# Optimization experiments

Hardware: AMD Instinct MI355X
Metric: run time of the kernel (lower is better)

Reference implementation:

```python
import jax, jax.numpy as jnp
import numpy as np

BIG = 1e9
GRAPH_LAYERS = 2
FLOW_ITERS = 10
DUAL_ITERS = 10
STEP = 0.1
MOM = 0.9


def _forward(node_features, node_embeddings, demands, adj, neighborhoods,
             enc_W0, enc_b0, enc_W1, enc_b1,
             attn_W, attn_a_src, attn_a_dst, nbr_q,
             gru_W, gru_U, gru_b,
             dec_W0, dec_b0, dec_W1, dec_b1,
             dual_W0, dual_b0, dual_W1, dual_b1):
    E = enc_W1.shape[1]
    K = neighborhoods.shape[0]
    # --- node encoder MLP (tanh, activate_final=True) ---
    x = jnp.concatenate([node_embeddings, node_features], axis=-1)  # [B,N,Fin]
    h = jnp.tanh(jnp.tanh(x @ enc_W0 + enc_b0) @ enc_W1 + enc_b1)   # [B,N,E]
    attn_coefs = None
    for _ in range(GRAPH_LAYERS):
        # --- AttentionNeighborhood: multi-head GAT per hop level, then attention over levels ---
        z = jnp.einsum('bnd,hde->hbne', h, attn_W)                   # [H,B,N,E]
        s_src = jnp.einsum('hbne,he->hbn', z, attn_a_src)
        s_dst = jnp.einsum('hbne,he->hbn', z, attn_a_dst)
        scores = jnp.tanh(s_src[:, :, :, None] + s_dst[:, :, None, :])  # [H,B,N,N]
        aggs = []
        for k in range(K):
            masked = jnp.where(neighborhoods[k][None] > 0, scores, -BIG)
            alpha = jax.nn.softmax(masked, axis=-1)                  # [H,B,N,N]
            agg = jnp.tanh(jnp.einsum('hbnm,hbme->hbne', alpha, z).mean(axis=0))  # heads averaged -> [B,N,E]
            aggs.append(agg)
        aggs = jnp.stack(aggs, axis=2)                               # [B,N,K,E]
        attn_coefs = jax.nn.softmax(jnp.tanh(jnp.einsum('bnke,e->bnk', aggs, nbr_q)), axis=-1)
        nxt = jnp.einsum('bnk,bnke->bne', attn_coefs, aggs)          # [B,N,E]
        # --- GRU state update (tanh activation) ---
        zr = jax.nn.sigmoid(nxt @ gru_W[:, :2 * E] + h @ gru_U[:, :2 * E] + gru_b[:2 * E])
        zg, r = zr[..., :E], zr[..., E:]
        h_tilde = jnp.tanh(nxt @ gru_W[:, 2 * E:] + (r * h) @ gru_U[:, 2 * E:] + gru_b[2 * E:])
        h = (1.0 - zg) * h + zg * h_tilde
    # --- flow-proportion decoder + masked softmax over neighbors ---
    node_weights = jnp.tanh(h @ dec_W0 + dec_b0) @ dec_W1 + dec_b1   # [B,N,1]
    pred = adj * jnp.swapaxes(node_weights, 1, 2)                    # adj * node_weights^T
    weights = -BIG * (1.0 - adj) + pred
    prop = jax.nn.softmax(weights, axis=-1)                          # [B,N,N]
    # --- iterative min-cost-flow solver ---
    def mcf_step(flow, _):
        inflow = flow.sum(axis=1)[:, :, None]                        # inflow_i = sum_j flow[j,i]
        return prop * jax.nn.relu(inflow - demands), None
    flow, _ = jax.lax.scan(mcf_step, jnp.zeros_like(prop), None, length=FLOW_ITERS)
    # should_correct_flows: cancel opposing flow on each edge pair
    flow = flow - adj * jnp.minimum(flow, jnp.swapaxes(flow, 1, 2))
    flow_cost = jnp.sum(flow * flow, axis=(1, 2))                    # square cost, per graph
    # --- dual decoder + projected momentum ascent dual-flow solver ---
    dual_vars = jnp.tanh(h @ dual_W0 + dual_b0) @ dual_W1 + dual_b1  # [B,N,1]
    dual_diff = adj * (dual_vars - jnp.swapaxes(dual_vars, 1, 2))    # [B,N,N]
    def dual_step(carry, _):
        y, m = carry
        g = 2.0 * y - dual_diff                                      # d/dy [y^2 - dual_diff*y]
        m = MOM * m + g
        y = adj * jax.nn.relu(y - STEP * m)
        return (y, m), None
    (dflow, _m), _ = jax.lax.scan(dual_step,
                                  (jnp.zeros_like(dual_diff), jnp.zeros_like(dual_diff)),
                                  None, length=DUAL_ITERS)
    dual_demand = jnp.sum(dual_vars * demands, axis=(1, 2))
    dual_cost = jnp.sum(dflow * dflow - dual_diff * dflow, axis=(1, 2)) - dual_demand
    return flow_cost - dual_cost                                     # primal-dual gap loss, [B]


def setup_inputs() -> dict:
    key = jax.random.key(0)
    ks = jax.random.split(key, 24)
    B, N, Femb, Ffeat, E, H = 2, 2048, 16, 2, 64, 2
    Fin = Femb + Ffeat
    node_embeddings = jax.random.normal(ks[0], (B, N, Femb), jnp.float32)
    node_features = jax.random.normal(ks[1], (B, N, Ffeat), jnp.float32)
    d = jax.random.normal(ks[2], (B, N, 1), jnp.float32) * 0.1
    demands = d - d.mean(axis=1, keepdims=True)                      # balanced demands
    eye = jnp.eye(N, dtype=jnp.float32)
    u = jax.random.uniform(ks[3], (B, N, N))
    adj = (u < 0.008).astype(jnp.float32) * (1.0 - eye)              # avg degree ~16
    a2 = (jnp.matmul(adj, adj) > 0).astype(jnp.float32) * (1.0 - eye)
    neighborhoods = jnp.stack([adj, a2], axis=0)                     # [K,B,N,N]
    def init(k, fan_in, shape):
        return jax.random.normal(k, shape, jnp.float32) / jnp.sqrt(float(fan_in))
    return {
        'node_features': node_features, 'node_embeddings': node_embeddings,
        'demands': demands, 'adj': adj, 'neighborhoods': neighborhoods,
        'enc_W0': init(ks[4], Fin, (Fin, 64)), 'enc_b0': jnp.zeros((64,)),
        'enc_W1': init(ks[5], 64, (64, E)), 'enc_b1': jnp.zeros((E,)),
        'attn_W': init(ks[6], E, (H, E, E)),
        'attn_a_src': init(ks[7], E, (H, E)), 'attn_a_dst': init(ks[8], E, (H, E)),
        'nbr_q': init(ks[9], E, (E,)),
        'gru_W': init(ks[10], E, (E, 3 * E)), 'gru_U': init(ks[11], E, (E, 3 * E)),
        'gru_b': jnp.zeros((3 * E,)),
        'dec_W0': init(ks[12], E, (E, 64)), 'dec_b0': jnp.zeros((64,)),
        'dec_W1': init(ks[13], 64, (64, 1)), 'dec_b1': jnp.zeros((1,)),
        'dual_W0': init(ks[14], E, (E, 64)), 'dual_b0': jnp.zeros((64,)),
        'dual_W1': init(ks[15], 64, (64, 1)), 'dual_b1': jnp.zeros((1,)),
    }


def reference(node_features, node_embeddings, demands, adj, neighborhoods,
              enc_W0, enc_b0, enc_W1, enc_b1,
              attn_W, attn_a_src, attn_a_dst, nbr_q,
              gru_W, gru_U, gru_b,
              dec_W0, dec_b0, dec_W1, dec_b1,
              dual_W0, dual_b0, dual_W1, dual_b1):
    return _forward(node_features, node_embeddings, demands, adj, neighborhoods,
                    enc_W0, enc_b0, enc_W1, enc_b1,
                    attn_W, attn_a_src, attn_a_dst, nbr_q,
                    gru_W, gru_U, gru_b,
                    dec_W0, dec_b0, dec_W1, dec_b1,
                    dual_W0, dual_b0, dual_W1, dual_b1)
```

## Files before the change

### kernel.cpp

```cpp
#include <hip/hip_runtime.h>

#define B_ 2
#define N_ 2048
#define E_ 64
#define FIN_ 18
#define ADJ_CAP 128
#define A2_CAP 1024
#define DR 16

__device__ __forceinline__ float wave_sum(float v) {
  #pragma unroll
  for (int o = 32; o > 0; o >>= 1) v += __shfl_xor(v, o);
  return v;
}
__device__ __forceinline__ float wave_max(float v) {
  #pragma unroll
  for (int o = 32; o > 0; o >>= 1) v = fmaxf(v, __shfl_xor(v, o));
  return v;
}
__device__ __forceinline__ void grp_reduce(float4& a) {
  #pragma unroll
  for (int o = 16; o <= 32; o <<= 1) {
    a.x += __shfl_xor(a.x, o); a.y += __shfl_xor(a.y, o);
    a.z += __shfl_xor(a.z, o); a.w += __shfl_xor(a.w, o);
  }
}

__global__ void k_csr(const float* __restrict__ nbhd, int* __restrict__ adj_idx,
                      int* __restrict__ adj_cnt, int* __restrict__ a2_idx,
                      int* __restrict__ a2_cnt, float* __restrict__ accum) {
  int wid = blockIdx.x * 4 + (threadIdx.x >> 6);
  int lane = threadIdx.x & 63;
  if (wid == 0 && lane < 8) accum[lane] = 0.f;
  int k = wid / (B_ * N_);
  int rem = wid - k * (B_ * N_);
  const float* row = nbhd + ((size_t)k * (B_ * N_) + rem) * N_;
  int cap = (k == 0) ? ADJ_CAP : A2_CAP;
  int* idx = ((k == 0) ? adj_idx : a2_idx) + (size_t)rem * cap;
  int* cntp = ((k == 0) ? adj_cnt : a2_cnt) + rem;
  int cnt = 0;
  unsigned long long below = (1ull << lane) - 1ull;
  for (int j0 = 0; j0 < N_; j0 += 256) {
    float4 v = ((const float4*)(row + j0))[lane];
    bool p0 = v.x > 0.f, p1 = v.y > 0.f, p2 = v.z > 0.f, p3 = v.w > 0.f;
    unsigned long long b0 = __ballot(p0), b1 = __ballot(p1),
                       b2 = __ballot(p2), b3 = __ballot(p3);
    int pos = cnt + __popcll(b0 & below) + __popcll(b1 & below) +
              __popcll(b2 & below) + __popcll(b3 & below);
    int base_j = j0 + lane * 4;
    if (p0) { if (pos < cap) idx[pos] = base_j;     pos++; }
    if (p1) { if (pos < cap) idx[pos] = base_j + 1; pos++; }
    if (p2) { if (pos < cap) idx[pos] = base_j + 2; pos++; }
    if (p3) { if (pos < cap) idx[pos] = base_j + 3; pos++; }
    cnt += __popcll(b0) + __popcll(b1) + __popcll(b2) + __popcll(b3);
  }
  if (lane == 0) *cntp = (cnt < cap) ? cnt : cap;
}

__global__ __launch_bounds__(256) void k_enc(
    const float* __restrict__ emb, const float* __restrict__ feat,
    const float* __restrict__ W0, const float* __restrict__ b0,
    const float* __restrict__ W1, const float* __restrict__ b1,
    float* __restrict__ h) {
  int tid = threadIdx.x, w = tid >> 6, j = tid & 63;
  int row0 = blockIdx.x * DR;
  __shared__ float XL[DR][FIN_];
  __shared__ float HID[DR][64];
  for (int t = tid; t < DR * FIN_; t += 256) {
    int r = t / FIN_, d = t - r * FIN_;
    int row = row0 + r;
    XL[r][d] = (d < 16) ? emb[(size_t)row * 16 + d] : feat[(size_t)row * 2 + (d - 16)];
  }
  __syncthreads();
  float acc[4];
  float b0j = b0[j];
  #pragma unroll
  for (int r = 0; r < 4; r++) acc[r] = b0j;
  #pragma unroll 2
  for (int d = 0; d < FIN_; d++) {
    float wv = W0[d * 64 + j];
    #pragma unroll
    for (int r = 0; r < 4; r++) acc[r] += XL[w * 4 + r][d] * wv;
  }
  #pragma unroll
  for (int r = 0; r < 4; r++) HID[w * 4 + r][j] = tanhf(acc[r]);
  float b1j = b1[j];
  #pragma unroll
  for (int r = 0; r < 4; r++) acc[r] = b1j;
  for (int dq = 0; dq < 16; dq++) {
    float w0 = W1[(4 * dq + 0) * 64 + j];
    float w1 = W1[(4 * dq + 1) * 64 + j];
    float w2 = W1[(4 * dq + 2) * 64 + j];
    float w3 = W1[(4 * dq + 3) * 64 + j];
    #pragma unroll
    for (int r = 0; r < 4; r++) {
      float4 x = ((const float4*)HID[w * 4 + r])[dq];
      acc[r] += x.x * w0 + x.y * w1 + x.z * w2 + x.w * w3;
    }
  }
  #pragma unroll
  for (int r = 0; r < 4; r++)
    h[(size_t)(row0 + w * 4 + r) * 64 + j] = tanhf(acc[r]);
}

__global__ __launch_bounds__(256) void k_z(
    const float* __restrict__ h, const float* __restrict__ attn_W,
    const float* __restrict__ a_src, const float* __restrict__ a_dst,
    float* __restrict__ z, float* __restrict__ ssrc2, float* __restrict__ sdst2) {
  int tid = threadIdx.x, w = tid >> 6, j = tid & 63;
  int head = w & 1, rbase = (w >> 1) * 8;
  int row0 = blockIdx.x * DR;
  __shared__ float HL[DR][64];
  for (int t = tid; t < DR * 64; t += 256) HL[t >> 6][t & 63] = h[(size_t)row0 * 64 + t];
  __syncthreads();
  const float* W = attn_W + head * 64 * 64;
  float acc[8];
  #pragma unroll
  for (int r = 0; r < 8; r++) acc[r] = 0.f;
  for (int dq = 0; dq < 16; dq++) {
    float w0 = W[(4 * dq + 0) * 64 + j];
    float w1 = W[(4 * dq + 1) * 64 + j];
    float w2 = W[(4 * dq + 2) * 64 + j];
    float w3 = W[(4 * dq + 3) * 64 + j];
    #pragma unroll
    for (int r = 0; r < 8; r++) {
      float4 x = ((const float4*)HL[rbase + r])[dq];
      acc[r] += x.x * w0 + x.y * w1 + x.z * w2 + x.w * w3;
    }
  }
  float as = a_src[head * 64 + j], ad = a_dst[head * 64 + j];
  #pragma unroll
  for (int r = 0; r < 8; r++) {
    int row = row0 + rbase + r;
    z[((size_t)head * (B_ * N_) + row) * 64 + j] = acc[r];
    float rs = wave_sum(acc[r] * as), rd = wave_sum(acc[r] * ad);
    if (j == 0) {
      ssrc2[(size_t)row * 2 + head] = rs;
      sdst2[(size_t)row * 2 + head] = rd;
    }
  }
}

__global__ __launch_bounds__(64) void k_agg_adj(
    const int* __restrict__ adj_idx, const int* __restrict__ adj_cnt,
    const float* __restrict__ z, const float* __restrict__ ssrc2,
    const float* __restrict__ sdst2, float* __restrict__ aggs) {
  int row = blockIdx.x;
  int lane = threadIdx.x;
  int b = row >> 11;
  int cnt = adj_cnt[row];
  const int* idx = adj_idx + (size_t)row * ADJ_CAP;
  float2 ss = ((const float2*)ssrc2)[row];
  const float2* sd = (const float2*)sdst2 + (size_t)b * N_;
  int col0 = 0, col1 = 0;
  float e00 = 0.f, e10 = 0.f, e01 = 0.f, e11 = 0.f;
  if (lane < cnt) {
    col0 = idx[lane]; float2 s = sd[col0];
    e00 = __expf(tanhf(ss.x + s.x)); e10 = __expf(tanhf(ss.y + s.y));
  }
  if (lane + 64 < cnt) {
    col1 = idx[lane + 64]; float2 s = sd[col1];
    e01 = __expf(tanhf(ss.x + s.x)); e11 = __expf(tanhf(ss.y + s.y));
  }
  float tot0 = wave_sum(e00 + e01), tot1 = wave_sum(e10 + e11);
  float inv0 = (tot0 > 0.f) ? 1.f / tot0 : 0.f;
  float inv1 = (tot1 > 0.f) ? 1.f / tot1 : 0.f;
  const float* z0 = z + (size_t)b * N_ * 64;
  const float* z1 = z + ((size_t)(B_ * N_) + b * N_) * 64;
  int g = lane >> 4, li = lane & 15;
  float4 a0 = {0.f, 0.f, 0.f, 0.f}, a1 = {0.f, 0.f, 0.f, 0.f};
  for (int j0 = 0; j0 < 64; j0 += 4) {
    if (j0 >= cnt) break;
    int j = j0 + g;
    int c = __shfl(col0, j);
    float e0 = __shfl(e00, j), e1 = __shfl(e10, j);
    if (j < cnt) {
      float4 v0 = ((const float4*)(z0 + (size_t)c * 64))[li];
      float4 v1 = ((const float4*)(z1 + (size_t)c * 64))[li];
      a0.x += e0 * v0.x; a0.y += e0 * v0.y; a0.z += e0 * v0.z; a0.w += e0 * v0.w;
      a1.x += e1 * v1.x; a1.y += e1 * v1.y; a1.z += e1 * v1.z; a1.w += e1 * v1.w;
    }
  }
  if (cnt > 64) {
    for (int j0 = 0; j0 < 64; j0 += 4) {
      if (64 + j0 >= cnt) break;
      int j = j0 + g;
      int c = __shfl(col1, j);
      float e0 = __shfl(e01, j), e1 = __shfl(e11, j);
      if (64 + j < cnt) {
        float4 v0 = ((const float4*)(z0 + (size_t)c * 64))[li];
        float4 v1 = ((const float4*)(z1 + (size_t)c * 64))[li];
        a0.x += e0 * v0.x; a0.y += e0 * v0.y; a0.z += e0 * v0.z; a0.w += e0 * v0.w;
        a1.x += e1 * v1.x; a1.y += e1 * v1.y; a1.z += e1 * v1.z; a1.w += e1 * v1.w;
      }
    }
  }
  grp_reduce(a0); grp_reduce(a1);
  if (g == 0) {
    float4 o;
    o.x = tanhf(0.5f * (a0.x * inv0 + a1.x * inv1));
    o.y = tanhf(0.5f * (a0.y * inv0 + a1.y * inv1));
    o.z = tanhf(0.5f * (a0.z * inv0 + a1.z * inv1));
    o.w = tanhf(0.5f * (a0.w * inv0 + a1.w * inv1));
    ((float4*)(aggs + ((size_t)row * 2 + 0) * 64))[li] = o;
  }
}

__global__ __launch_bounds__(256) void k_agg_a2(
    const int* __restrict__ a2_idx, const int* __restrict__ a2_cnt,
    const float* __restrict__ z, const float* __restrict__ ssrc2,
    const float* __restrict__ sdst2, float* __restrict__ aggs) {
  int row = blockIdx.x;
  int tid = threadIdx.x;
  int w = tid >> 6, lane = tid & 63;
  int b = row >> 11;
  int cnt = a2_cnt[row];
  const int* idx = a2_idx + (size_t)row * A2_CAP;
  float2 ss = ((const float2*)ssrc2)[row];
  const float2* sd = (const float2*)sdst2 + (size_t)b * N_;
  int colr[4]; float e0r[4], e1r[4];
  float s0 = 0.f, s1 = 0.f;
  #pragma unroll
  for (int c = 0; c < 4; c++) {
    int t = c * 256 + tid;
    colr[c] = 0; e0r[c] = 0.f; e1r[c] = 0.f;
    if (t < cnt) {
      int cc = idx[t]; colr[c] = cc;
      float2 s = sd[cc];
      e0r[c] = __expf(tanhf(ss.x + s.x));
      e1r[c] = __expf(tanhf(ss.y + s.y));
      s0 += e0r[c]; s1 += e1r[c];
    }
  }
  s0 = wave_sum(s0); s1 = wave_sum(s1);
  __shared__ float RED[2][4];
  __shared__ float WS0[4][64], WS1[4][64];
  if (lane == 0) { RED[0][w] = s0; RED[1][w] = s1; }
  const float* z0 = z + (size_t)b * N_ * 64;
  const float* z1 = z + ((size_t)(B_ * N_) + b * N_) * 64;
  int g = lane >> 4, li = lane & 15;
  float4 a0 = {0.f, 0.f, 0.f, 0.f}, a1 = {0.f, 0.f, 0.f, 0.f};
  #pragma unroll
  for (int c = 0; c < 4; c++) {
    int base = c * 256 + w * 64;
    if (base >= cnt) break;
    for (int j0 = 0; j0 < 64; j0 += 4) {
      if (base + j0 >= cnt) break;
      int j = j0 + g;
      int col = __shfl(colr[c], j);
      float e0 = __shfl(e0r[c], j), e1 = __shfl(e1r[c], j);
      if (base + j < cnt) {
        float4 v0 = ((const float4*)(z0 + (size_t)col * 64))[li];
        float4 v1 = ((const float4*)(z1 + (size_t)col * 64))[li];
        a0.x += e0 * v0.x; a0.y += e0 * v0.y; a0.z += e0 * v0.z; a0.w += e0 * v0.w;
        a1.x += e1 * v1.x; a1.y += e1 * v1.y; a1.z += e1 * v1.z; a1.w += e1 * v1.w;
      }
    }
  }
  grp_reduce(a0); grp_reduce(a1);
  if (g == 0) {
    ((float4*)WS0[w])[li] = a0;
    ((float4*)WS1[w])[li] = a1;
  }
  __syncthreads();
  if (tid < 64) {
    float tot0 = RED[0][0] + RED[0][1] + RED[0][2] + RED[0][3];
    float tot1 = RED[1][0] + RED[1][1] + RED[1][2] + RED[1][3];
    float inv0 = (tot0 > 0.f) ? 1.f / tot0 : 0.f;
    float inv1 = (tot1 > 0.f) ? 1.f / tot1 : 0.f;
    float r0 = WS0[0][tid] + WS0[1][tid] + WS0[2][tid] + WS0[3][tid];
    float r1 = WS1[0][tid] + WS1[1][tid] + WS1[2][tid] + WS1[3][tid];
    aggs[((size_t)row * 2 + 1) * 64 + tid] = tanhf(0.5f * (r0 * inv0 + r1 * inv1));
  }
}

__global__ __launch_bounds__(256) void k_comb(
    const float* __restrict__ aggs, const float* __restrict__ nbr_q,
    const float* __restrict__ gru_W, const float* __restrict__ gru_U,
    const float* __restrict__ gru_b, float* __restrict__ h) {
  int tid = threadIdx.x, w = tid >> 6, j = tid & 63;
  int row0 = blockIdx.x * DR;
  __shared__ float HL[DR][64], NL[DR][64], RGL[DR][64];
  for (int t = tid; t < DR * 64; t += 256) HL[t >> 6][t & 63] = h[(size_t)row0 * 64 + t];
  float q = nbr_q[j];
  #pragma unroll
  for (int r = 0; r < 4; r++) {
    int rr = w * 4 + r, row = row0 + rr;
    float a0 = aggs[((size_t)row * 2 + 0) * 64 + j];
    float a1 = aggs[((size_t)row * 2 + 1) * 64 + j];
    float t0 = tanhf(wave_sum(a0 * q));
    float t1 = tanhf(wave_sum(a1 * q));
    float mx = fmaxf(t0, t1);
    float e0 = __expf(t0 - mx), e1 = __expf(t1 - mx);
    float inv = 1.f / (e0 + e1);
    NL[rr][j] = (e0 * a0 + e1 * a1) * inv;
  }
  __syncthreads();
  float az[4], ar[4];
  float bz = gru_b[j], br = gru_b[64 + j];
  #pragma unroll
  for (int r = 0; r < 4; r++) { az[r] = bz; ar[r] = br; }
  for (int dq = 0; dq < 16; dq++) {
    int d0 = 4 * dq;
    float wz0 = gru_W[(d0 + 0) * 192 + j],      wz1 = gru_W[(d0 + 1) * 192 + j];
    float wz2 = gru_W[(d0 + 2) * 192 + j],      wz3 = gru_W[(d0 + 3) * 192 + j];
    float wr0 = gru_W[(d0 + 0) * 192 + 64 + j], wr1 = gru_W[(d0 + 1) * 192 + 64 + j];
    float wr2 = gru_W[(d0 + 2) * 192 + 64 + j], wr3 = gru_W[(d0 + 3) * 192 + 64 + j];
    float uz0 = gru_U[(d0 + 0) * 192 + j],      uz1 = gru_U[(d0 + 1) * 192 + j];
    float uz2 = gru_U[(d0 + 2) * 192 + j],      uz3 = gru_U[(d0 + 3) * 192 + j];
    float ur0 = gru_U[(d0 + 0) * 192 + 64 + j], ur1 = gru_U[(d0 + 1) * 192 + 64 + j];
    float ur2 = gru_U[(d0 + 2) * 192 + 64 + j], ur3 = gru_U[(d0 + 3) * 192 + 64 + j];
    #pragma unroll
    for (int r = 0; r < 4; r++) {
      float4 n = ((const float4*)NL[w * 4 + r])[dq];
      float4 x = ((const float4*)HL[w * 4 + r])[dq];
      az[r] += n.x * wz0 + n.y * wz1 + n.z * wz2 + n.w * wz3
             + x.x * uz0 + x.y * uz1 + x.z * uz2 + x.w * uz3;
      ar[r] += n.x * wr0 + n.y * wr1 + n.z * wr2 + n.w * wr3
             + x.x * ur0 + x.y * ur1 + x.z * ur2 + x.w * ur3;
    }
  }
  float zgr[4];
  #pragma unroll
  for (int r = 0; r < 4; r++) {
    zgr[r] = 1.f / (1.f + __expf(-az[r]));
    RGL[w * 4 + r][j] = 1.f / (1.f + __expf(-ar[r]));
  }
  float ah[4];
  float bh = gru_b[128 + j];
  #pragma unroll
  for (int r = 0; r < 4; r++) ah[r] = bh;
  for (int dq = 0; dq < 16; dq++) {
    int d0 = 4 * dq;
    float wh0 = gru_W[(d0 + 0) * 192 + 128 + j], wh1 = gru_W[(d0 + 1) * 192 + 128 + j];
    float wh2 = gru_W[(d0 + 2) * 192 + 128 + j], wh3 = gru_W[(d0 + 3) * 192 + 128 + j];
    float uh0 = gru_U[(d0 + 0) * 192 + 128 + j], uh1 = gru_U[(d0 + 1) * 192 + 128 + j];
    float uh2 = gru_U[(d0 + 2) * 192 + 128 + j], uh3 = gru_U[(d0 + 3) * 192 + 128 + j];
    #pragma unroll
    for (int r = 0; r < 4; r++) {
      float4 n = ((const float4*)NL[w * 4 + r])[dq];
      float4 x = ((const float4*)HL[w * 4 + r])[dq];
      float4 rg = ((const float4*)RGL[w * 4 + r])[dq];
      ah[r] += n.x * wh0 + n.y * wh1 + n.z * wh2 + n.w * wh3
             + rg.x * x.x * uh0 + rg.y * x.y * uh1
             + rg.z * x.z * uh2 + rg.w * x.w * uh3;
    }
  }
  #pragma unroll
  for (int r = 0; r < 4; r++) {
    int rr = w * 4 + r;
    float ht = tanhf(ah[r]);
    float hj = HL[rr][j];
    h[(size_t)(row0 + rr) * 64 + j] = (1.f - zgr[r]) * hj + zgr[r] * ht;
  }
}

__global__ __launch_bounds__(256) void k_dec(
    const float* __restrict__ h, const float* __restrict__ dW0,
    const float* __restrict__ db0, const float* __restrict__ dW1,
    const float* __restrict__ db1, const float* __restrict__ uW0,
    const float* __restrict__ ub0, const float* __restrict__ uW1,
    const float* __restrict__ ub1, const float* __restrict__ demands,
    float* __restrict__ nw, float* __restrict__ dv, float* accum) {
  int tid = threadIdx.x, w = tid >> 6, j = tid & 63;
  int row0 = blockIdx.x * DR;
  __shared__ float HL[DR][64];
  __shared__ float DD[4];
  for (int t = tid; t < DR * 64; t += 256) HL[t >> 6][t & 63] = h[(size_t)row0 * 64 + t];
  __syncthreads();
  float accd[4], accu[4];
  float db0j = db0[j], ub0j = ub0[j];
  #pragma unroll
  for (int r = 0; r < 4; r++) { accd[r] = db0j; accu[r] = ub0j; }
  for (int dq = 0; dq < 16; dq++) {
    int d0 = 4 * dq;
    float dw0 = dW0[(d0 + 0) * 64 + j], dw1 = dW0[(d0 + 1) * 64 + j];
    float dw2 = dW0[(d0 + 2) * 64 + j], dw3 = dW0[(d0 + 3) * 64 + j];
    float uw0 = uW0[(d0 + 0) * 64 + j], uw1 = uW0[(d0 + 1) * 64 + j];
    float uw2 = uW0[(d0 + 2) * 64 + j], uw3 = uW0[(d0 + 3) * 64 + j];
    #pragma unroll
    for (int r = 0; r < 4; r++) {
      float4 x = ((const float4*)HL[w * 4 + r])[dq];
      accd[r] += x.x * dw0 + x.y * dw1 + x.z * dw2 + x.w * dw3;
      accu[r] += x.x * uw0 + x.y * uw1 + x.z * uw2 + x.w * uw3;
    }
  }
  float dw1c = dW1[j], uw1c = uW1[j];
  float db1s = db1[0], ub1s = ub1[0];
  float ddl = 0.f;
  #pragma unroll
  for (int r = 0; r < 4; r++) {
    int row = row0 + w * 4 + r;
    float a = wave_sum(tanhf(accd[r]) * dw1c);
    float bb = wave_sum(tanhf(accu[r]) * uw1c);
    if (j == 0) {
      float dvv = bb + ub1s;
      nw[row] = a + db1s; dv[row] = dvv;
      ddl += dvv * demands[row];
    }
  }
  if (j == 0) DD[w] = ddl;
  __syncthreads();
  if (tid == 0) atomicAdd(&accum[4 + (row0 >> 11)], DD[0] + DD[1] + DD[2] + DD[3]);
}

__global__ void k_prop(const int* __restrict__ adj_idx, const int* __restrict__ adj_cnt,
                       const float* __restrict__ nw, float* __restrict__ Pval,
                       int* __restrict__ tcnt) {
  int row = blockIdx.x;
  int lane = threadIdx.x;
  int b = row >> 11;
  int cnt = adj_cnt[row];
  const int* idx = adj_idx + (size_t)row * ADJ_CAP;
  int c0 = (lane < cnt) ? idx[lane] : -1;
  int c1 = (lane + 64 < cnt) ? idx[lane + 64] : -1;
  float v0 = (c0 >= 0) ? nw[b * N_ + c0] : -1e30f;
  float v1 = (c1 >= 0) ? nw[b * N_ + c1] : -1e30f;
  float m = wave_max(fmaxf(v0, v1));
  float e0 = (c0 >= 0) ? __expf(v0 - m) : 0.f;
  float e1 = (c1 >= 0) ? __expf(v1 - m) : 0.f;
  float s = wave_sum(e0 + e1);
  float inv = (s > 0.f) ? 1.f / s : 0.f;
  if (c0 >= 0) Pval[(size_t)row * ADJ_CAP + lane] = e0 * inv;
  if (c1 >= 0) Pval[(size_t)row * ADJ_CAP + lane + 64] = e1 * inv;
  if (lane == 0) tcnt[row] = 0;
}

__global__ void k_transpose(const int* __restrict__ adj_idx, const int* __restrict__ adj_cnt,
                            const float* __restrict__ Pval, int* __restrict__ tcnt,
                            int* __restrict__ tsrc, float* __restrict__ tval) {
  int row = blockIdx.x;
  int lane = threadIdx.x;
  int cnt = adj_cnt[row];
  int base = row & ~(N_ - 1);
  for (int t = lane; t < cnt; t += 64) {
    int j = adj_idx[(size_t)row * ADJ_CAP + t];
    int col = base + j;
    int pos = atomicAdd(&tcnt[col], 1);
    if (pos < ADJ_CAP) {
      tsrc[(size_t)col * ADJ_CAP + pos] = row;
      tval[(size_t)col * ADJ_CAP + pos] = Pval[(size_t)row * ADJ_CAP + t];
    }
  }
}

__global__ __launch_bounds__(1024) void k_mcf_all(
    const int* __restrict__ tcnt, const int* __restrict__ tsrc,
    const float* __restrict__ tval, const float* __restrict__ demands,
    float* __restrict__ s_out) {
  int b = blockIdx.x, tid = threadIdx.x;
  __shared__ float SBUF[2][N_];
  __shared__ float DL[N_];
  for (int i = tid; i < N_; i += 1024) {
    float d = demands[b * N_ + i];
    DL[i] = d;
    SBUF[0][i] = fmaxf(-d, 0.f);
  }
  __syncthreads();
  int cur = 0;
  for (int it = 0; it < 9; it++) {
    const float* Sin = SBUF[cur];
    float* Sout = SBUF[cur ^ 1];
    for (int i = tid; i < N_; i += 1024) {
      int gi = b * N_ + i;
      int cnt = tcnt[gi];
      const int* src = tsrc + (size_t)gi * ADJ_CAP;
      const float* val = tval + (size_t)gi * ADJ_CAP;
      float c = 0.f;
      int c4 = cnt >> 2;
      for (int qq = 0; qq < c4; qq++) {
        int4 s4 = ((const int4*)src)[qq];
        float4 v4 = ((const float4*)val)[qq];
        c += v4.x * Sin[s4.x & (N_ - 1)] + v4.y * Sin[s4.y & (N_ - 1)]
           + v4.z * Sin[s4.z & (N_ - 1)] + v4.w * Sin[s4.w & (N_ - 1)];
      }
      for (int t = c4 * 4; t < cnt; t++) c += val[t] * Sin[src[t] & (N_ - 1)];
      Sout[i] = fmaxf(c - DL[i], 0.f);
    }
    __syncthreads();
    cur ^= 1;
  }
  for (int i = tid; i < N_; i += 1024) s_out[b * N_ + i] = SBUF[cur][i];
}

__global__ __launch_bounds__(256) void k_flowdual(
    const int* __restrict__ adj_idx, const int* __restrict__ adj_cnt,
    const float* __restrict__ Pval, const float* __restrict__ s,
    const float* __restrict__ dv, float* accum) {
  int tid = threadIdx.x;
  int lane = tid & 63, w = tid >> 6;
  int r16 = lane >> 4, e = lane & 15;
  int row = blockIdx.x * 16 + w * 4 + r16;
  int b = row >> 11, i = row & (N_ - 1);
  int cnt = adj_cnt[row];
  float si = s[row], dvi = dv[row];
  const int* idx = adj_idx + (size_t)row * ADJ_CAP;
  const float* pv = Pval + (size_t)row * ADJ_CAP;
  float fc = 0.f, dc = 0.f;
  for (int t = e; t < cnt; t += 16) {
    int j = idx[t];
    float f_ij = si * pv[t];
    const int* jidx = adj_idx + (size_t)(b * N_ + j) * ADJ_CAP;
    int jcnt = adj_cnt[b * N_ + j];
    int lo = 0, hi = jcnt, pos = -1;
    while (lo < hi) {
      int mid = (lo + hi) >> 1;
      int v = jidx[mid];
      if (v == i) { pos = mid; break; }
      if (v < i) lo = mid + 1; else hi = mid;
    }
    float f_ji = (pos >= 0) ? s[b * N_ + j] * Pval[(size_t)(b * N_ + j) * ADJ_CAP + pos] : 0.f;
    float fin = f_ij - fminf(f_ij, f_ji);
    fc += fin * fin;
    float dd = dvi - dv[b * N_ + j];
    float y = 0.f, m = 0.f;
    #pragma unroll
    for (int q = 0; q < 10; q++) {
      float g = 2.f * y - dd;
      m = 0.9f * m + g;
      y = fmaxf(y - 0.1f * m, 0.f);
    }
    dc += y * y - dd * y;
  }
  fc = wave_sum(fc); dc = wave_sum(dc);
  __shared__ float FB[4], DB[4];
  if (lane == 0) { FB[w] = fc; DB[w] = dc; }
  __syncthreads();
  if (tid == 0) {
    int bb = (blockIdx.x * 16) >> 11;
    atomicAdd(&accum[bb], FB[0] + FB[1] + FB[2] + FB[3]);
    atomicAdd(&accum[2 + bb], DB[0] + DB[1] + DB[2] + DB[3]);
  }
}

__global__ void k_fin(const float* accum, float* out) {
  int b = threadIdx.x;
  if (b < B_) out[b] = accum[b] - accum[2 + b] + accum[4 + b];
}

extern "C" void kernel_launch(void* const* d_in, const int* in_sizes, int n_in,
                              void* d_out, int out_size, void* d_ws, size_t ws_size,
                              hipStream_t stream) {
  const float* feat    = (const float*)d_in[0];
  const float* emb     = (const float*)d_in[1];
  const float* demands = (const float*)d_in[2];
  const float* nbhd    = (const float*)d_in[4];
  const float* enc_W0  = (const float*)d_in[5];
  const float* enc_b0  = (const float*)d_in[6];
  const float* enc_W1  = (const float*)d_in[7];
  const float* enc_b1  = (const float*)d_in[8];
  const float* attn_W  = (const float*)d_in[9];
  const float* a_src   = (const float*)d_in[10];
  const float* a_dst   = (const float*)d_in[11];
  const float* nbr_q   = (const float*)d_in[12];
  const float* gru_W   = (const float*)d_in[13];
  const float* gru_U   = (const float*)d_in[14];
  const float* gru_b   = (const float*)d_in[15];
  const float* dec_W0  = (const float*)d_in[16];
  const float* dec_b0  = (const float*)d_in[17];
  const float* dec_W1  = (const float*)d_in[18];
  const float* dec_b1  = (const float*)d_in[19];
  const float* dual_W0 = (const float*)d_in[20];
  const float* dual_b0 = (const float*)d_in[21];
  const float* dual_W1 = (const float*)d_in[22];
  const float* dual_b1 = (const float*)d_in[23];
  float* out = (float*)d_out;

  char* ws = (char*)d_ws;
  size_t off = 0;
  auto alloc = [&](size_t bytes) { char* p = ws + off; off += (bytes + 255) & ~(size_t)255; return p; };
  int*   adj_idx = (int*)  alloc((size_t)B_ * N_ * ADJ_CAP * 4);
  int*   adj_cnt = (int*)  alloc((size_t)B_ * N_ * 4);
  int*   a2_idx  = (int*)  alloc((size_t)B_ * N_ * A2_CAP * 4);
  int*   a2_cnt  = (int*)  alloc((size_t)B_ * N_ * 4);
  float* h       = (float*)alloc((size_t)B_ * N_ * 64 * 4);
  float* z       = (float*)alloc((size_t)2 * B_ * N_ * 64 * 4);
  float* ssrc2   = (float*)alloc((size_t)2 * B_ * N_ * 4);
  float* sdst2   = (float*)alloc((size_t)2 * B_ * N_ * 4);
  float* aggs    = (float*)alloc((size_t)B_ * N_ * 2 * 64 * 4);
  float* nw      = (float*)alloc((size_t)B_ * N_ * 4);
  float* dv      = (float*)alloc((size_t)B_ * N_ * 4);
  float* Pval    = (float*)alloc((size_t)B_ * N_ * ADJ_CAP * 4);
  int*   tcnt    = (int*)  alloc((size_t)B_ * N_ * 4);
  int*   tsrc    = (int*)  alloc((size_t)B_ * N_ * ADJ_CAP * 4);
  float* tval    = (float*)alloc((size_t)B_ * N_ * ADJ_CAP * 4);
  float* s_final = (float*)alloc((size_t)B_ * N_ * 4);
  float* accum   = (float*)alloc(8 * 4);

  k_csr<<<(2 * B_ * N_) / 4, 256, 0, stream>>>(nbhd, adj_idx, adj_cnt, a2_idx, a2_cnt, accum);
  k_enc<<<(B_ * N_) / DR, 256, 0, stream>>>(emb, feat, enc_W0, enc_b0, enc_W1, enc_b1, h);
  for (int layer = 0; layer < 2; layer++) {
    k_z<<<(B_ * N_) / DR, 256, 0, stream>>>(h, attn_W, a_src, a_dst, z, ssrc2, sdst2);
    k_agg_adj<<<B_ * N_, 64, 0, stream>>>(adj_idx, adj_cnt, z, ssrc2, sdst2, aggs);
    k_agg_a2<<<B_ * N_, 256, 0, stream>>>(a2_idx, a2_cnt, z, ssrc2, sdst2, aggs);
    k_comb<<<(B_ * N_) / DR, 256, 0, stream>>>(aggs, nbr_q, gru_W, gru_U, gru_b, h);
  }
  k_dec<<<(B_ * N_) / DR, 256, 0, stream>>>(h, dec_W0, dec_b0, dec_W1, dec_b1,
                                            dual_W0, dual_b0, dual_W1, dual_b1,
                                            demands, nw, dv, accum);
  k_prop<<<B_ * N_, 64, 0, stream>>>(adj_idx, adj_cnt, nw, Pval, tcnt);
  k_transpose<<<B_ * N_, 64, 0, stream>>>(adj_idx, adj_cnt, Pval, tcnt, tsrc, tval);
  k_mcf_all<<<B_, 1024, 0, stream>>>(tcnt, tsrc, tval, demands, s_final);
  k_flowdual<<<(B_ * N_) / 16, 256, 0, stream>>>(adj_idx, adj_cnt, Pval, s_final, dv, accum);
  k_fin<<<1, 64, 0, stream>>>(accum, out);
}
```

Baseline: 434.6 us.

## Fuse prop+transpose and split MCF iterations into grid-wide kernel launches

Folds the transpose scatter into the softmax-proportion kernel and moves tcnt zeroing into the CSR build kernel, which removes one launch and a reread of Pval. The MCF fixed-point iteration previously ran in two 1024-thread blocks using shared memory. It now runs as 9 separate launches of 16 blocks each, with the state ping-ponging through global buffers. This spreads the gather work over more CUs at the cost of extra launches and global-memory traffic for the state vector.

```diff
diff --git a/kernel.cpp b/kernel.cpp
--- a/kernel.cpp
+++ b/kernel.cpp
@@ -28,12 +28,14 @@
 
 __global__ void k_csr(const float* __restrict__ nbhd, int* __restrict__ adj_idx,
                       int* __restrict__ adj_cnt, int* __restrict__ a2_idx,
-                      int* __restrict__ a2_cnt, float* __restrict__ accum) {
+                      int* __restrict__ a2_cnt, float* __restrict__ accum,
+                      int* __restrict__ tcnt) {
   int wid = blockIdx.x * 4 + (threadIdx.x >> 6);
   int lane = threadIdx.x & 63;
   if (wid == 0 && lane < 8) accum[lane] = 0.f;
   int k = wid / (B_ * N_);
   int rem = wid - k * (B_ * N_);
+  if (k == 0 && lane == 0) tcnt[rem] = 0;
   const float* row = nbhd + ((size_t)k * (B_ * N_) + rem) * N_;
   int cap = (k == 0) ? ADJ_CAP : A2_CAP;
   int* idx = ((k == 0) ? adj_idx : a2_idx) + (size_t)rem * cap;
@@ -404,83 +406,65 @@
   if (tid == 0) atomicAdd(&accum[4 + (row0 >> 11)], DD[0] + DD[1] + DD[2] + DD[3]);
 }
 
-__global__ void k_prop(const int* __restrict__ adj_idx, const int* __restrict__ adj_cnt,
-                       const float* __restrict__ nw, float* __restrict__ Pval,
-                       int* __restrict__ tcnt) {
+__global__ void k_propT(const int* __restrict__ adj_idx, const int* __restrict__ adj_cnt,
+                        const float* __restrict__ nw, const float* __restrict__ demands,
+                        float* __restrict__ Pval, int* __restrict__ tcnt,
+                        int* __restrict__ tsrc, float* __restrict__ tval,
+                        float* __restrict__ sA) {
   int row = blockIdx.x;
   int lane = threadIdx.x;
   int b = row >> 11;
+  int base = b * N_;
   int cnt = adj_cnt[row];
   const int* idx = adj_idx + (size_t)row * ADJ_CAP;
   int c0 = (lane < cnt) ? idx[lane] : -1;
   int c1 = (lane + 64 < cnt) ? idx[lane + 64] : -1;
-  float v0 = (c0 >= 0) ? nw[b * N_ + c0] : -1e30f;
-  float v1 = (c1 >= 0) ? nw[b * N_ + c1] : -1e30f;
+  float v0 = (c0 >= 0) ? nw[base + c0] : -1e30f;
+  float v1 = (c1 >= 0) ? nw[base + c1] : -1e30f;
   float m = wave_max(fmaxf(v0, v1));
   float e0 = (c0 >= 0) ? __expf(v0 - m) : 0.f;
   float e1 = (c1 >= 0) ? __expf(v1 - m) : 0.f;
   float s = wave_sum(e0 + e1);
   float inv = (s > 0.f) ? 1.f / s : 0.f;
-  if (c0 >= 0) Pval[(size_t)row * ADJ_CAP + lane] = e0 * inv;
-  if (c1 >= 0) Pval[(size_t)row * ADJ_CAP + lane + 64] = e1 * inv;
-  if (lane == 0) tcnt[row] = 0;
-}
-
-__global__ void k_transpose(const int* __restrict__ adj_idx, const int* __restrict__ adj_cnt,
-                            const float* __restrict__ Pval, int* __restrict__ tcnt,
-                            int* __restrict__ tsrc, float* __restrict__ tval) {
-  int row = blockIdx.x;
-  int lane = threadIdx.x;
-  int cnt = adj_cnt[row];
-  int base = row & ~(N_ - 1);
-  for (int t = lane; t < cnt; t += 64) {
-    int j = adj_idx[(size_t)row * ADJ_CAP + t];
-    int col = base + j;
+  float p0 = e0 * inv, p1 = e1 * inv;
+  if (c0 >= 0) {
+    Pval[(size_t)row * ADJ_CAP + lane] = p0;
+    int col = base + c0;
     int pos = atomicAdd(&tcnt[col], 1);
     if (pos < ADJ_CAP) {
       tsrc[(size_t)col * ADJ_CAP + pos] = row;
-      tval[(size_t)col * ADJ_CAP + pos] = Pval[(size_t)row * ADJ_CAP + t];
-    }
-  }
-}
-
-__global__ __launch_bounds__(1024) void k_mcf_all(
+      tval[(size_t)col * ADJ_CAP + pos] = p0;
+    }
+  }
+  if (c1 >= 0) {
+    Pval[(size_t)row * ADJ_CAP + lane + 64] = p1;
+    int col = base + c1;
+    int pos = atomicAdd(&tcnt[col], 1);
+    if (pos < ADJ_CAP) {
+      tsrc[(size_t)col * ADJ_CAP + pos] = row;
+      tval[(size_t)col * ADJ_CAP + pos] = p1;
+    }
+  }
+  if (lane == 0) sA[row] = fmaxf(-demands[row], 0.f);
+}
+
+__global__ __launch_bounds__(256) void k_mcf_iter(
     const int* __restrict__ tcnt, const int* __restrict__ tsrc,
     const float* __restrict__ tval, const float* __restrict__ demands,
-    float* __restrict__ s_out) {
-  int b = blockIdx.x, tid = threadIdx.x;
-  __shared__ float SBUF[2][N_];
-  __shared__ float DL[N_];
-  for (int i = tid; i < N_; i += 1024) {
-    float d = demands[b * N_ + i];
-    DL[i] = d;
-    SBUF[0][i] = fmaxf(-d, 0.f);
-  }
-  __syncthreads();
-  int cur = 0;
-  for (int it = 0; it < 9; it++) {
-    const float* Sin = SBUF[cur];
-    float* Sout = SBUF[cur ^ 1];
-    for (int i = tid; i < N_; i += 1024) {
-      int gi = b * N_ + i;
-      int cnt = tcnt[gi];
-      const int* src = tsrc + (size_t)gi * ADJ_CAP;
-      const float* val = tval + (size_t)gi * ADJ_CAP;
-      float c = 0.f;
-      int c4 = cnt >> 2;
-      for (int qq = 0; qq < c4; qq++) {
-        int4 s4 = ((const int4*)src)[qq];
-        float4 v4 = ((const float4*)val)[qq];
-        c += v4.x * Sin[s4.x & (N_ - 1)] + v4.y * Sin[s4.y & (N_ - 1)]
-           + v4.z * Sin[s4.z & (N_ - 1)] + v4.w * Sin[s4.w & (N_ - 1)];
-      }
-      for (int t = c4 * 4; t < cnt; t++) c += val[t] * Sin[src[t] & (N_ - 1)];
-      Sout[i] = fmaxf(c - DL[i], 0.f);
-    }
-    __syncthreads();
-    cur ^= 1;
-  }
-  for (int i = tid; i < N_; i += 1024) s_out[b * N_ + i] = SBUF[cur][i];
+    const float* __restrict__ s_in, float* __restrict__ s_out) {
+  int j = blockIdx.x * 256 + threadIdx.x;
+  int cnt = tcnt[j];
+  const int* src = tsrc + (size_t)j * ADJ_CAP;
+  const float* val = tval + (size_t)j * ADJ_CAP;
+  float c = 0.f;
+  int c4 = cnt >> 2;
+  for (int q = 0; q < c4; q++) {
+    int4 s4 = ((const int4*)src)[q];
+    float4 v4 = ((const float4*)val)[q];
+    c += v4.x * s_in[s4.x] + v4.y * s_in[s4.y] + v4.z * s_in[s4.z] + v4.w * s_in[s4.w];
+  }
+  for (int t = c4 * 4; t < cnt; t++) c += val[t] * s_in[src[t]];
+  s_out[j] = fmaxf(c - demands[j], 0.f);
 }
 
 __global__ __launch_bounds__(256) void k_flowdual(
@@ -584,10 +568,12 @@
   int*   tcnt    = (int*)  alloc((size_t)B_ * N_ * 4);
   int*   tsrc    = (int*)  alloc((size_t)B_ * N_ * ADJ_CAP * 4);
   float* tval    = (float*)alloc((size_t)B_ * N_ * ADJ_CAP * 4);
-  float* s_final = (float*)alloc((size_t)B_ * N_ * 4);
+  float* sA      = (float*)alloc((size_t)B_ * N_ * 4);
+  float* sB      = (float*)alloc((size_t)B_ * N_ * 4);
   float* accum   = (float*)alloc(8 * 4);
 
-  k_csr<<<(2 * B_ * N_) / 4, 256, 0, stream>>>(nbhd, adj_idx, adj_cnt, a2_idx, a2_cnt, accum);
+  k_csr<<<(2 * B_ * N_) / 4, 256, 0, stream>>>(nbhd, adj_idx, adj_cnt, a2_idx, a2_cnt,
+                                               accum, tcnt);
   k_enc<<<(B_ * N_) / DR, 256, 0, stream>>>(emb, feat, enc_W0, enc_b0, enc_W1, enc_b1, h);
   for (int layer = 0; layer < 2; layer++) {
     k_z<<<(B_ * N_) / DR, 256, 0, stream>>>(h, attn_W, a_src, a_dst, z, ssrc2, sdst2);
@@ -598,9 +584,13 @@
   k_dec<<<(B_ * N_) / DR, 256, 0, stream>>>(h, dec_W0, dec_b0, dec_W1, dec_b1,
                                             dual_W0, dual_b0, dual_W1, dual_b1,
                                             demands, nw, dv, accum);
-  k_prop<<<B_ * N_, 64, 0, stream>>>(adj_idx, adj_cnt, nw, Pval, tcnt);
-  k_transpose<<<B_ * N_, 64, 0, stream>>>(adj_idx, adj_cnt, Pval, tcnt, tsrc, tval);
-  k_mcf_all<<<B_, 1024, 0, stream>>>(tcnt, tsrc, tval, demands, s_final);
-  k_flowdual<<<(B_ * N_) / 16, 256, 0, stream>>>(adj_idx, adj_cnt, Pval, s_final, dv, accum);
+  k_propT<<<B_ * N_, 64, 0, stream>>>(adj_idx, adj_cnt, nw, demands, Pval,
+                                      tcnt, tsrc, tval, sA);
+  for (int it = 0; it < 9; it++) {
+    float* sin  = (it & 1) ? sB : sA;
+    float* sout = (it & 1) ? sA : sB;
+    k_mcf_iter<<<(B_ * N_) / 256, 256, 0, stream>>>(tcnt, tsrc, tval, demands, sin, sout);
+  }
+  k_flowdual<<<(B_ * N_) / 16, 256, 0, stream>>>(adj_idx, adj_cnt, Pval, sB, dv, accum);
   k_fin<<<1, 64, 0, stream>>>(accum, out);
 }
```

After: 385.4 us. 11.3% less time.
